# Kernel optimization log

Measured on AMD Instinct MI355X. Metric: run time of the kernel, lower is better.

Reference implementation:

```python
import jax, jax.numpy as jnp
import numpy as np

B, W, F = 64, 128, 64          # batch, window (node feat dim), n_features (nodes)
H, OUTW = 4, 128               # num_heads, out window size
NEG_SLOPE = 0.2                # LeakyReLU negative slope (alpha)


def setup_inputs() -> dict:
    key = jax.random.key(0)
    ks = jax.random.split(key, 6)
    scale_in = 1.0 / np.sqrt(W)
    scale_a = 1.0 / np.sqrt(OUTW)
    return {
        "x": jax.random.normal(ks[0], (B, W, F), dtype=jnp.float32),
        "W_src": jax.random.normal(ks[1], (H * OUTW, W), dtype=jnp.float32) * scale_in,
        "b_src": jnp.zeros((H * OUTW,), dtype=jnp.float32),
        "W_dst": jax.random.normal(ks[2], (H * OUTW, W), dtype=jnp.float32) * scale_in,
        "b_dst": jnp.zeros((H * OUTW,), dtype=jnp.float32),
        "attn": jax.random.normal(ks[3], (H, OUTW), dtype=jnp.float32) * scale_a,
    }


def reference(x, W_src, b_src, W_dst, b_dst, attn):
    # x: [B, W, F] -> node features nf: [B, F, W] (F nodes, W-dim features)
    nf = jnp.transpose(x, (0, 2, 1))
    b, f, w = nf.shape
    h, outw = attn.shape
    # GATv2 separate source/destination projections (share_weights=False)
    fs = (nf @ W_src.T + b_src).reshape(b, f, h, outw)  # [B, F, H, outW]
    fd = (nf @ W_dst.T + b_dst).reshape(b, f, h, outw)
    # additive score over complete graph with self-loops: e[b,i,j,h,d]
    s = fs[:, :, None, :, :] + fd[:, None, :, :, :]      # [B, src, dst, H, outW]
    e = jnp.where(s >= 0, s, NEG_SLOPE * s)              # LeakyReLU
    scores = jnp.einsum('bijhd,hd->bhij', e, attn)       # [B, H, src, dst]
    # edge softmax: normalize over incoming edges (sources) per destination
    a = jax.nn.softmax(scores, axis=2)
    # weighted scatter-sum aggregation at destinations
    out = jnp.einsum('bhij,bihd->bjhd', a, fs)           # [B, F, H, outW]
    out = out.mean(axis=2)                               # mean over heads -> [B, F, outW]
    return jnp.transpose(out, (0, 2, 1))                 # [B, outW, F]
```

## Files before the change

### kernel.cpp

```cpp
#include <hip/hip_runtime.h>
#include <math.h>

#define BB 64
#define WW 128
#define FF 64
#define HH 4
#define OW 128

__global__ __launch_bounds__(256) void gat_proj(
    const float* __restrict__ x,
    const float* __restrict__ Wsrc,
    const float* __restrict__ bsrc,
    const float* __restrict__ Wdst,
    const float* __restrict__ bdst,
    float* __restrict__ fs,
    float* __restrict__ fd)
{
    __shared__ float xl[64 * FF];
    __shared__ float wl[64 * 68];
    __shared__ float bl[64];

    const int b  = blockIdx.x >> 4;
    const int rt = blockIdx.x & 15;
    const bool is_src = rt < 8;
    const int rm0 = (rt & 7) * 64;

    const float* Wm = is_src ? Wsrc : Wdst;
    const float* bm = is_src ? bsrc : bdst;

    const int t  = threadIdx.x;
    const int f0 = (t & 15) * 4;
    const int r0 = (t >> 4) * 4;

    float acc[4][4] = {};

    for (int kp = 0; kp < 2; ++kp) {
        {
            const float4* xs = (const float4*)(x + (size_t)b * (WW * FF) + kp * 64 * FF);
            float4* xd = (float4*)xl;
            #pragma unroll
            for (int p = 0; p < 4; ++p)
                xd[p * 256 + t] = xs[p * 256 + t];
            float4* wd = (float4*)wl;
            #pragma unroll
            for (int p = 0; p < 4; ++p) {
                int idx = p * 256 + t;
                int r = idx >> 4, kq = idx & 15;
                wd[r * 17 + kq] =
                    *(const float4*)(Wm + (size_t)(rm0 + r) * WW + kp * 64 + kq * 4);
            }
            if (kp == 0 && t < 64) bl[t] = bm[rm0 + t];
        }
        __syncthreads();

        #pragma unroll
        for (int k0 = 0; k0 < 64; k0 += 4) {
            float4 xv[4], wv[4];
            #pragma unroll
            for (int kk = 0; kk < 4; ++kk)
                xv[kk] = *(const float4*)&xl[(k0 + kk) * FF + f0];
            #pragma unroll
            for (int rr = 0; rr < 4; ++rr)
                wv[rr] = *(const float4*)&wl[(r0 + rr) * 68 + k0];
            #pragma unroll
            for (int kk = 0; kk < 4; ++kk) {
                #pragma unroll
                for (int rr = 0; rr < 4; ++rr) {
                    const float wf = ((const float*)&wv[rr])[kk];
                    const float* xf = (const float*)&xv[kk];
                    acc[rr][0] = fmaf(xf[0], wf, acc[rr][0]);
                    acc[rr][1] = fmaf(xf[1], wf, acc[rr][1]);
                    acc[rr][2] = fmaf(xf[2], wf, acc[rr][2]);
                    acc[rr][3] = fmaf(xf[3], wf, acc[rr][3]);
                }
            }
        }
        __syncthreads();
    }

    const int h  = (rt & 7) >> 1;
    const int d0 = ((rt & 1) * 64) + r0;
    float* dst = (is_src ? fs : fd) + (((size_t)b * HH + h) * FF) * OW;
    float b0 = bl[r0 + 0], b1 = bl[r0 + 1], b2 = bl[r0 + 2], b3 = bl[r0 + 3];
    #pragma unroll
    for (int ff = 0; ff < 4; ++ff) {
        float4 o;
        o.x = acc[0][ff] + b0;
        o.y = acc[1][ff] + b1;
        o.z = acc[2][ff] + b2;
        o.w = acc[3][ff] + b3;
        *(float4*)&dst[(size_t)(f0 + ff) * OW + d0] = o;
    }
}

__global__ __launch_bounds__(256) void gat_attn(
    const float* __restrict__ fs,
    const float* __restrict__ fd,
    const float* __restrict__ attn,
    float* __restrict__ ws2)
{
    __shared__ float fsl[FF * 132];
    __shared__ float fdl[32 * 132];
    __shared__ float St[FF * 36];
    __shared__ float A6[OW], B4[OW];
    __shared__ float cs[FF], cd[32];
    __shared__ float redm[8][32];
    __shared__ float reds[8][32];
    __shared__ float invl[32];

    const int bx = blockIdx.x;
    const int jh = bx & 1;
    const int h  = (bx >> 1) & 3;
    const int b  = bx >> 3;
    const size_t bh = (size_t)b * HH + h;
    const int jbase = jh * 32;

    const int t    = threadIdx.x;
    const int wv   = t >> 6;
    const int lane = t & 63;

    {
        const float4* s = (const float4*)(fs + bh * (FF * OW));
        float4* d4 = (float4*)fsl;
        #pragma unroll
        for (int p = 0; p < 8; ++p) {
            int idx = p * 256 + t;
            int i = idx >> 5, kq = idx & 31;
            d4[i * 33 + kq] = s[idx];
        }
        const float4* fsrc = (const float4*)(fd + (bh * FF + jbase) * OW);
        float4* fdst = (float4*)fdl;
        #pragma unroll
        for (int p = 0; p < 4; ++p) {
            int idx = p * 256 + t;
            int j = idx >> 5, kq = idx & 31;
            fdst[j * 33 + kq] = fsrc[idx];
        }
        if (t < 128) {
            float a = attn[h * OW + t];
            A6[t] = 0.6f * a;
            B4[t] = 0.4f * a;
        }
    }
    __syncthreads();

    if (t < 64) {
        float s = 0.0f;
        #pragma unroll 8
        for (int c = 0; c < 32; ++c) {
            float4 fv = *(const float4*)&fsl[t * 132 + c * 4];
            float4 av = *(const float4*)&A6[c * 4];
            s = fmaf(fv.x, av.x, fmaf(fv.y, av.y, fmaf(fv.z, av.z, fmaf(fv.w, av.w, s))));
        }
        cs[t] = s;
    } else if (t < 96) {
        const int j = t - 64;
        float s = 0.0f;
        #pragma unroll 8
        for (int c = 0; c < 32; ++c) {
            float4 fv = *(const float4*)&fdl[j * 132 + c * 4];
            float4 av = *(const float4*)&A6[c * 4];
            s = fmaf(fv.x, av.x, fmaf(fv.y, av.y, fmaf(fv.z, av.z, fmaf(fv.w, av.w, s))));
        }
        cd[j] = s;
    }
    __syncthreads();

    const int jl0 = wv * 8;
    {
        float sc[8] = {};
        #pragma unroll 4
        for (int c = 0; c < 32; ++c) {
            const int d0 = c * 4;
            float4 fsv = *(const float4*)&fsl[lane * 132 + d0];
            float4 b4  = *(const float4*)&B4[d0];
            #pragma unroll
            for (int jj = 0; jj < 8; ++jj) {
                float4 fdv = *(const float4*)&fdl[(jl0 + jj) * 132 + d0];
                float r = sc[jj];
                r = fmaf(b4.x, fabsf(fsv.x + fdv.x), r);
                r = fmaf(b4.y, fabsf(fsv.y + fdv.y), r);
                r = fmaf(b4.z, fabsf(fsv.z + fdv.z), r);
                r = fmaf(b4.w, fabsf(fsv.w + fdv.w), r);
                sc[jj] = r;
            }
        }
        const float csl = cs[lane];
        float4 o0, o1;
        o0.x = sc[0] + csl + cd[jl0 + 0];
        o0.y = sc[1] + csl + cd[jl0 + 1];
        o0.z = sc[2] + csl + cd[jl0 + 2];
        o0.w = sc[3] + csl + cd[jl0 + 3];
        o1.x = sc[4] + csl + cd[jl0 + 4];
        o1.y = sc[5] + csl + cd[jl0 + 5];
        o1.z = sc[6] + csl + cd[jl0 + 6];
        o1.w = sc[7] + csl + cd[jl0 + 7];
        *(float4*)&St[lane * 36 + jl0]     = o0;
        *(float4*)&St[lane * 36 + jl0 + 4] = o1;
    }
    __syncthreads();

    {
        const int j = t & 31, st = t >> 5;
        const int i0 = st * 8;
        float m = St[i0 * 36 + j];
        #pragma unroll
        for (int k = 1; k < 8; ++k) m = fmaxf(m, St[(i0 + k) * 36 + j]);
        redm[st][j] = m;
    }
    __syncthreads();
    {
        const int j = t & 31, st = t >> 5;
        const int i0 = st * 8;
        float mj = redm[0][j];
        #pragma unroll
        for (int s2 = 1; s2 < 8; ++s2) mj = fmaxf(mj, redm[s2][j]);
        float ps = 0.0f;
        #pragma unroll
        for (int k = 0; k < 8; ++k) {
            float e = __expf(St[(i0 + k) * 36 + j] - mj);
            St[(i0 + k) * 36 + j] = e;
            ps += e;
        }
        reds[st][j] = ps;
    }
    __syncthreads();
    if (t < 32) {
        float l = 0.0f;
        #pragma unroll
        for (int s2 = 0; s2 < 8; ++s2) l += reds[s2][t];
        invl[t] = 0.25f / l;
    }
    __syncthreads();

    {
        const int dg = t & 7;
        const int jr = t >> 3;
        float ag[16] = {};
        for (int i = 0; i < FF; ++i) {
            const float p = St[i * 36 + jr];
            const float* fr = &fsl[i * 132 + dg * 4];
            float4 f0 = *(const float4*)(fr);
            float4 f1 = *(const float4*)(fr + 32);
            float4 f2 = *(const float4*)(fr + 64);
            float4 f3 = *(const float4*)(fr + 96);
            ag[0]  = fmaf(p, f0.x, ag[0]);  ag[1]  = fmaf(p, f0.y, ag[1]);
            ag[2]  = fmaf(p, f0.z, ag[2]);  ag[3]  = fmaf(p, f0.w, ag[3]);
            ag[4]  = fmaf(p, f1.x, ag[4]);  ag[5]  = fmaf(p, f1.y, ag[5]);
            ag[6]  = fmaf(p, f1.z, ag[6]);  ag[7]  = fmaf(p, f1.w, ag[7]);
            ag[8]  = fmaf(p, f2.x, ag[8]);  ag[9]  = fmaf(p, f2.y, ag[9]);
            ag[10] = fmaf(p, f2.z, ag[10]); ag[11] = fmaf(p, f2.w, ag[11]);
            ag[12] = fmaf(p, f3.x, ag[12]); ag[13] = fmaf(p, f3.y, ag[13]);
            ag[14] = fmaf(p, f3.z, ag[14]); ag[15] = fmaf(p, f3.w, ag[15]);
        }
        const float iv = invl[jr];
        float* wout = ws2 + (bh * FF + jbase + jr) * OW + dg * 4;
        #pragma unroll
        for (int q = 0; q < 4; ++q) {
            float4 o;
            o.x = ag[q * 4 + 0] * iv;
            o.y = ag[q * 4 + 1] * iv;
            o.z = ag[q * 4 + 2] * iv;
            o.w = ag[q * 4 + 3] * iv;
            *(float4*)&wout[q * 32] = o;
        }
    }
}

__global__ __launch_bounds__(256) void gat_reduce(
    const float* __restrict__ ws2,
    float* __restrict__ out)
{
    __shared__ float tl[16][132];
    const int b  = blockIdx.x >> 2;
    const int jg = blockIdx.x & 3;
    const int t  = threadIdx.x;

    const float* base = ws2 + ((size_t)b * HH * FF + jg * 16) * OW;
    #pragma unroll
    for (int p = 0; p < 2; ++p) {
        int idx = p * 256 + t;
        int j = idx >> 5, q = idx & 31;
        const float* src = base + (size_t)j * OW + q * 4;
        float4 s0 = *(const float4*)(src);
        float4 s1 = *(const float4*)(src + (size_t)FF * OW);
        float4 s2 = *(const float4*)(src + (size_t)2 * FF * OW);
        float4 s3 = *(const float4*)(src + (size_t)3 * FF * OW);
        float4 o;
        o.x = s0.x + s1.x + s2.x + s3.x;
        o.y = s0.y + s1.y + s2.y + s3.y;
        o.z = s0.z + s1.z + s2.z + s3.z;
        o.w = s0.w + s1.w + s2.w + s3.w;
        *(float4*)&tl[j][q * 4] = o;
    }
    __syncthreads();
    #pragma unroll
    for (int it = 0; it < 8; ++it) {
        int idx = it * 256 + t;
        int j = idx & 15, d = idx >> 4;
        out[((size_t)b * OW + d) * FF + jg * 16 + j] = tl[j][d];
    }
}

extern "C" void kernel_launch(void* const* d_in, const int* in_sizes, int n_in,
                              void* d_out, int out_size, void* d_ws, size_t ws_size,
                              hipStream_t stream) {
    const float* x    = (const float*)d_in[0];
    const float* Wsrc = (const float*)d_in[1];
    const float* bsrc = (const float*)d_in[2];
    const float* Wdst = (const float*)d_in[3];
    const float* bdst = (const float*)d_in[4];
    const float* attn = (const float*)d_in[5];
    float* out = (float*)d_out;

    const size_t SL = (size_t)BB * HH * FF * OW;
    float* fs  = (float*)d_ws;
    float* fd  = fs + SL;
    float* ws2 = fd + SL;

    gat_proj  <<<BB * 16,     256, 0, stream>>>(x, Wsrc, bsrc, Wdst, bdst, fs, fd);
    gat_attn  <<<BB * HH * 2, 256, 0, stream>>>(fs, fd, attn, ws2);
    gat_reduce<<<BB * 4,      256, 0, stream>>>(ws2, out);
}
```

Before: 115.5 us.

## Fuse head reduction into attention kernel with atomics and retile score loop

Each attention block now covers a whole (batch, head) pair with 512 threads instead of half the destinations. It writes head-averaged results straight into the output through global atomicAdd after a memset, which removes the ws2 workspace and the separate reduce kernel. The score loop is retiled so each thread keeps a 32-dim slice of the transposed fd in registers and combines partial sums via shared-memory atomics. The cost is extra memset and atomic traffic, plus non-deterministic float summation order.

```diff
diff --git a/kernel.cpp b/kernel.cpp
--- a/kernel.cpp
+++ b/kernel.cpp
@@ -93,48 +93,46 @@
     }
 }
 
-__global__ __launch_bounds__(256) void gat_attn(
+__global__ __launch_bounds__(512, 2) void gat_attn(
     const float* __restrict__ fs,
     const float* __restrict__ fd,
     const float* __restrict__ attn,
-    float* __restrict__ ws2)
+    float* __restrict__ out)
 {
     __shared__ float fsl[FF * 132];
-    __shared__ float fdl[32 * 132];
-    __shared__ float St[FF * 36];
+    __shared__ float fdt[OW * 68];
+    __shared__ float St[FF * 68];
     __shared__ float A6[OW], B4[OW];
-    __shared__ float cs[FF], cd[32];
-    __shared__ float redm[8][32];
-    __shared__ float reds[8][32];
-    __shared__ float invl[32];
-
-    const int bx = blockIdx.x;
-    const int jh = bx & 1;
-    const int h  = (bx >> 1) & 3;
-    const int b  = bx >> 3;
+    __shared__ float cs[FF], cd[FF];
+    __shared__ float redm[8][FF];
+    __shared__ float reds[8][FF];
+    __shared__ float invl[FF];
+
+    const int h = blockIdx.x & 3;
+    const int b = blockIdx.x >> 2;
     const size_t bh = (size_t)b * HH + h;
-    const int jbase = jh * 32;
 
     const int t    = threadIdx.x;
     const int wv   = t >> 6;
     const int lane = t & 63;
 
     {
-        const float4* s = (const float4*)(fs + bh * (FF * OW));
-        float4* d4 = (float4*)fsl;
-        #pragma unroll
-        for (int p = 0; p < 8; ++p) {
-            int idx = p * 256 + t;
+        const float4* s4 = (const float4*)(fs + bh * (FF * OW));
+        #pragma unroll
+        for (int p = 0; p < 4; ++p) {
+            int idx = p * 512 + t;
             int i = idx >> 5, kq = idx & 31;
-            d4[i * 33 + kq] = s[idx];
-        }
-        const float4* fsrc = (const float4*)(fd + (bh * FF + jbase) * OW);
-        float4* fdst = (float4*)fdl;
+            *(float4*)&fsl[i * 132 + kq * 4] = s4[idx];
+        }
+        const float* fdg = fd + bh * (FF * OW);
         #pragma unroll
         for (int p = 0; p < 4; ++p) {
-            int idx = p * 256 + t;
-            int j = idx >> 5, kq = idx & 31;
-            fdst[j * 33 + kq] = fsrc[idx];
+            int dq = p * 8 + wv;
+            float4 v = *(const float4*)(fdg + (size_t)lane * OW + dq * 4);
+            fdt[(dq * 4 + 0) * 68 + lane] = v.x;
+            fdt[(dq * 4 + 1) * 68 + lane] = v.y;
+            fdt[(dq * 4 + 2) * 68 + lane] = v.z;
+            fdt[(dq * 4 + 3) * 68 + lane] = v.w;
         }
         if (t < 128) {
             float a = attn[h * OW + t];
@@ -144,73 +142,88 @@
     }
     __syncthreads();
 
-    if (t < 64) {
+    if (wv == 0) {
         float s = 0.0f;
         #pragma unroll 8
         for (int c = 0; c < 32; ++c) {
-            float4 fv = *(const float4*)&fsl[t * 132 + c * 4];
+            float4 fv = *(const float4*)&fsl[lane * 132 + c * 4];
             float4 av = *(const float4*)&A6[c * 4];
             s = fmaf(fv.x, av.x, fmaf(fv.y, av.y, fmaf(fv.z, av.z, fmaf(fv.w, av.w, s))));
         }
-        cs[t] = s;
-    } else if (t < 96) {
-        const int j = t - 64;
+        cs[lane] = s;
+    } else if (wv == 1) {
         float s = 0.0f;
-        #pragma unroll 8
-        for (int c = 0; c < 32; ++c) {
-            float4 fv = *(const float4*)&fdl[j * 132 + c * 4];
-            float4 av = *(const float4*)&A6[c * 4];
-            s = fmaf(fv.x, av.x, fmaf(fv.y, av.y, fmaf(fv.z, av.z, fmaf(fv.w, av.w, s))));
-        }
-        cd[j] = s;
-    }
-    __syncthreads();
-
-    const int jl0 = wv * 8;
-    {
-        float sc[8] = {};
+        #pragma unroll 16
+        for (int d = 0; d < OW; ++d)
+            s = fmaf(fdt[d * 68 + lane], A6[d], s);
+        cd[lane] = s;
+    }
+    __syncthreads();
+
+    {
+        const int i = t >> 3, jb = (t & 7) * 8;
+        const float ci = cs[i];
+        float4 c0 = *(const float4*)&cd[jb];
+        float4 c1 = *(const float4*)&cd[jb + 4];
+        float4 o0 = {ci + c0.x, ci + c0.y, ci + c0.z, ci + c0.w};
+        float4 o1 = {ci + c1.x, ci + c1.y, ci + c1.z, ci + c1.w};
+        *(float4*)&St[i * 68 + jb]     = o0;
+        *(float4*)&St[i * 68 + jb + 4] = o1;
+    }
+    __syncthreads();
+
+    {
+        const int ie = t >> 7;
+        const int dh = (t >> 5) & 3;
+        const int jp = t & 31;
+        const int i0 = ie * 16, d0 = dh * 32, j0 = jp * 2;
+
+        float4 b4r[8];
+        #pragma unroll
+        for (int q = 0; q < 8; ++q) b4r[q] = *(const float4*)&B4[d0 + q * 4];
+        float2 fdr[32];
+        #pragma unroll
+        for (int dd = 0; dd < 32; ++dd)
+            fdr[dd] = *(const float2*)&fdt[(d0 + dd) * 68 + j0];
+
+        float sc0[16], sc1[16];
         #pragma unroll 4
-        for (int c = 0; c < 32; ++c) {
-            const int d0 = c * 4;
-            float4 fsv = *(const float4*)&fsl[lane * 132 + d0];
-            float4 b4  = *(const float4*)&B4[d0];
-            #pragma unroll
-            for (int jj = 0; jj < 8; ++jj) {
-                float4 fdv = *(const float4*)&fdl[(jl0 + jj) * 132 + d0];
-                float r = sc[jj];
-                r = fmaf(b4.x, fabsf(fsv.x + fdv.x), r);
-                r = fmaf(b4.y, fabsf(fsv.y + fdv.y), r);
-                r = fmaf(b4.z, fabsf(fsv.z + fdv.z), r);
-                r = fmaf(b4.w, fabsf(fsv.w + fdv.w), r);
-                sc[jj] = r;
-            }
-        }
-        const float csl = cs[lane];
-        float4 o0, o1;
-        o0.x = sc[0] + csl + cd[jl0 + 0];
-        o0.y = sc[1] + csl + cd[jl0 + 1];
-        o0.z = sc[2] + csl + cd[jl0 + 2];
-        o0.w = sc[3] + csl + cd[jl0 + 3];
-        o1.x = sc[4] + csl + cd[jl0 + 4];
-        o1.y = sc[5] + csl + cd[jl0 + 5];
-        o1.z = sc[6] + csl + cd[jl0 + 6];
-        o1.w = sc[7] + csl + cd[jl0 + 7];
-        *(float4*)&St[lane * 36 + jl0]     = o0;
-        *(float4*)&St[lane * 36 + jl0 + 4] = o1;
-    }
-    __syncthreads();
-
-    {
-        const int j = t & 31, st = t >> 5;
+        for (int ii = 0; ii < 16; ++ii) {
+            const float* fr = &fsl[(i0 + ii) * 132 + d0];
+            float a0 = 0.0f, a1 = 0.0f;
+            #pragma unroll
+            for (int q = 0; q < 8; ++q) {
+                float4 fsv = *(const float4*)(fr + q * 4);
+                const float* fe = (const float*)&fsv;
+                const float* be = (const float*)&b4r[q];
+                #pragma unroll
+                for (int e = 0; e < 4; ++e) {
+                    const float fv = fe[e];
+                    a0 = fmaf(be[e], fabsf(fv + fdr[q * 4 + e].x), a0);
+                    a1 = fmaf(be[e], fabsf(fv + fdr[q * 4 + e].y), a1);
+                }
+            }
+            sc0[ii] = a0; sc1[ii] = a1;
+        }
+        #pragma unroll
+        for (int ii = 0; ii < 16; ++ii) {
+            atomicAdd(&St[(i0 + ii) * 68 + j0],     sc0[ii]);
+            atomicAdd(&St[(i0 + ii) * 68 + j0 + 1], sc1[ii]);
+        }
+    }
+    __syncthreads();
+
+    {
+        const int j = t & 63, st = t >> 6;
         const int i0 = st * 8;
-        float m = St[i0 * 36 + j];
-        #pragma unroll
-        for (int k = 1; k < 8; ++k) m = fmaxf(m, St[(i0 + k) * 36 + j]);
+        float m = St[i0 * 68 + j];
+        #pragma unroll
+        for (int k = 1; k < 8; ++k) m = fmaxf(m, St[(i0 + k) * 68 + j]);
         redm[st][j] = m;
     }
     __syncthreads();
     {
-        const int j = t & 31, st = t >> 5;
+        const int j = t & 63, st = t >> 6;
         const int i0 = st * 8;
         float mj = redm[0][j];
         #pragma unroll
@@ -218,14 +231,14 @@
         float ps = 0.0f;
         #pragma unroll
         for (int k = 0; k < 8; ++k) {
-            float e = __expf(St[(i0 + k) * 36 + j] - mj);
-            St[(i0 + k) * 36 + j] = e;
+            float e = __expf(St[(i0 + k) * 68 + j] - mj);
+            St[(i0 + k) * 68 + j] = e;
             ps += e;
         }
         reds[st][j] = ps;
     }
     __syncthreads();
-    if (t < 32) {
+    if (t < 64) {
         float l = 0.0f;
         #pragma unroll
         for (int s2 = 0; s2 < 8; ++s2) l += reds[s2][t];
@@ -234,71 +247,30 @@
     __syncthreads();
 
     {
-        const int dg = t & 7;
-        const int jr = t >> 3;
-        float ag[16] = {};
+        const int jg = t & 15, dg = t >> 4;
+        const int j0 = jg * 4, d0 = dg * 4;
+        float ag[4][4] = {};
+        #pragma unroll 4
         for (int i = 0; i < FF; ++i) {
-            const float p = St[i * 36 + jr];
-            const float* fr = &fsl[i * 132 + dg * 4];
-            float4 f0 = *(const float4*)(fr);
-            float4 f1 = *(const float4*)(fr + 32);
-            float4 f2 = *(const float4*)(fr + 64);
-            float4 f3 = *(const float4*)(fr + 96);
-            ag[0]  = fmaf(p, f0.x, ag[0]);  ag[1]  = fmaf(p, f0.y, ag[1]);
-            ag[2]  = fmaf(p, f0.z, ag[2]);  ag[3]  = fmaf(p, f0.w, ag[3]);
-            ag[4]  = fmaf(p, f1.x, ag[4]);  ag[5]  = fmaf(p, f1.y, ag[5]);
-            ag[6]  = fmaf(p, f1.z, ag[6]);  ag[7]  = fmaf(p, f1.w, ag[7]);
-            ag[8]  = fmaf(p, f2.x, ag[8]);  ag[9]  = fmaf(p, f2.y, ag[9]);
-            ag[10] = fmaf(p, f2.z, ag[10]); ag[11] = fmaf(p, f2.w, ag[11]);
-            ag[12] = fmaf(p, f3.x, ag[12]); ag[13] = fmaf(p, f3.y, ag[13]);
-            ag[14] = fmaf(p, f3.z, ag[14]); ag[15] = fmaf(p, f3.w, ag[15]);
-        }
-        const float iv = invl[jr];
-        float* wout = ws2 + (bh * FF + jbase + jr) * OW + dg * 4;
-        #pragma unroll
-        for (int q = 0; q < 4; ++q) {
-            float4 o;
-            o.x = ag[q * 4 + 0] * iv;
-            o.y = ag[q * 4 + 1] * iv;
-            o.z = ag[q * 4 + 2] * iv;
-            o.w = ag[q * 4 + 3] * iv;
-            *(float4*)&wout[q * 32] = o;
-        }
-    }
-}
-
-__global__ __launch_bounds__(256) void gat_reduce(
-    const float* __restrict__ ws2,
-    float* __restrict__ out)
-{
-    __shared__ float tl[16][132];
-    const int b  = blockIdx.x >> 2;
-    const int jg = blockIdx.x & 3;
-    const int t  = threadIdx.x;
-
-    const float* base = ws2 + ((size_t)b * HH * FF + jg * 16) * OW;
-    #pragma unroll
-    for (int p = 0; p < 2; ++p) {
-        int idx = p * 256 + t;
-        int j = idx >> 5, q = idx & 31;
-        const float* src = base + (size_t)j * OW + q * 4;
-        float4 s0 = *(const float4*)(src);
-        float4 s1 = *(const float4*)(src + (size_t)FF * OW);
-        float4 s2 = *(const float4*)(src + (size_t)2 * FF * OW);
-        float4 s3 = *(const float4*)(src + (size_t)3 * FF * OW);
-        float4 o;
-        o.x = s0.x + s1.x + s2.x + s3.x;
-        o.y = s0.y + s1.y + s2.y + s3.y;
-        o.z = s0.z + s1.z + s2.z + s3.z;
-        o.w = s0.w + s1.w + s2.w + s3.w;
-        *(float4*)&tl[j][q * 4] = o;
-    }
-    __syncthreads();
-    #pragma unroll
-    for (int it = 0; it < 8; ++it) {
-        int idx = it * 256 + t;
-        int j = idx & 15, d = idx >> 4;
-        out[((size_t)b * OW + d) * FF + jg * 16 + j] = tl[j][d];
+            float4 pv = *(const float4*)&St[i * 68 + j0];
+            float4 fv = *(const float4*)&fsl[i * 132 + d0];
+            const float* pf = (const float*)&pv;
+            const float* fe = (const float*)&fv;
+            #pragma unroll
+            for (int n = 0; n < 4; ++n) {
+                #pragma unroll
+                for (int e = 0; e < 4; ++e)
+                    ag[n][e] = fmaf(pf[n], fe[e], ag[n][e]);
+            }
+        }
+        float* ob = out + (size_t)b * (OW * FF);
+        #pragma unroll
+        for (int n = 0; n < 4; ++n) {
+            const float iv = invl[j0 + n];
+            #pragma unroll
+            for (int e = 0; e < 4; ++e)
+                atomicAdd(&ob[(size_t)(d0 + e) * FF + j0 + n], ag[n][e] * iv);
+        }
     }
 }
 
@@ -314,11 +286,10 @@
     float* out = (float*)d_out;
 
     const size_t SL = (size_t)BB * HH * FF * OW;
-    float* fs  = (float*)d_ws;
-    float* fd  = fs + SL;
-    float* ws2 = fd + SL;
-
-    gat_proj  <<<BB * 16,     256, 0, stream>>>(x, Wsrc, bsrc, Wdst, bdst, fs, fd);
-    gat_attn  <<<BB * HH * 2, 256, 0, stream>>>(fs, fd, attn, ws2);
-    gat_reduce<<<BB * 4,      256, 0, stream>>>(ws2, out);
+    float* fs = (float*)d_ws;
+    float* fd = fs + SL;
+
+    hipMemsetAsync(out, 0, (size_t)out_size * sizeof(float), stream);
+    gat_proj<<<BB * 16, 256, 0, stream>>>(x, Wsrc, bsrc, Wdst, bdst, fs, fd);
+    gat_attn<<<BB * HH, 512, 0, stream>>>(fs, fd, attn, out);
 }
```

After: 148.2 us. +28.3%, slower.
